# Optimization experiments

Measured on AMD Instinct MI355X. Metric: run time of the kernel, lower is better.

The kernel has to match this reference:

```python
import jax, jax.numpy as jnp
import numpy as np

T = 4096          # batch_size (time points)
C = 4096          # input_dims[1] == num_filters (channels/neurons)
FW = 64           # filter_width (temporal taps)


def setup_inputs() -> dict:
    key = jax.random.key(0)
    k1, k2, k3 = jax.random.split(key, 3)
    inputs = jax.random.normal(k1, (T, C), dtype=jnp.float32)
    weights = jax.random.uniform(k2, (FW, C), dtype=jnp.float32)
    biases = jax.random.normal(k3, (C,), dtype=jnp.float32) * 0.01
    return {"inputs": inputs, "weights": weights, "biases": biases}


def reference(inputs, weights, biases):
    # weight-norm (normalize_weights=1): per-filter L2 over taps, floored at 1e-8
    wnorms = jnp.maximum(jnp.sqrt(jnp.sum(jnp.square(weights), axis=0)), 1e-8)  # [C]
    filt = jnp.maximum(0.0, weights / wnorms)  # pos_constraint clamp, [FW, C]
    # Original does a full conv2d -> [C, T, 1, C] then takes the diagonal over
    # (batch-channel, filter-channel). Mathematically this is a per-channel
    # depthwise temporal SAME conv (cross-correlation, matching tf.nn.conv2d).
    x = inputs.T[None, :, :]            # [1, C, T]  (NCH)
    k = filt.T[:, None, :]              # [C, 1, FW] (OIH), group size 1
    pre = jax.lax.conv_general_dilated(
        x, k, window_strides=(1,), padding="SAME",
        feature_group_count=C,
        dimension_numbers=("NCH", "OIH", "NCH"))  # [1, C, T]
    # bias add; activation 'lin' = identity; ei_mask is None (num_inh=0)
    out = pre[0].T + biases[None, :]    # [T, C]
    return out
```

## Files before the change

### kernel.cpp

```cpp
#include <hip/hip_runtime.h>


#define T_DIM 4096
#define C_DIM 4096
#define PAD_L 31
#define KTILE 128

template <bool GUARD>
__device__ __forceinline__ void fir_body(const float* __restrict__ x,
                                         const float* __restrict__ w,
                                         const float* __restrict__ b,
                                         float* __restrict__ out,
                                         int c, int t0) {
    const float* __restrict__ xp = x + c;
    float* __restrict__ op = out + (long long)t0 * C_DIM + c;

    float wf[64];
    float ss = 0.0f;
#pragma unroll
    for (int f = 0; f < 64; ++f) {
        wf[f] = w[f * C_DIM + c];
        ss = fmaf(wf[f], wf[f], ss);
    }
    const float inv = 1.0f / fmaxf(sqrtf(ss), 1e-8f);
#pragma unroll
    for (int f = 0; f < 64; ++f) wf[f] = fmaxf(wf[f] * inv, 0.0f);

    const float bv = b[c];
    const int base = t0 - PAD_L;

#define LOADX(m) ((!GUARD || ((unsigned)(m) < (unsigned)T_DIM))               \
                      ? xp[(long long)(m) * C_DIM] : 0.0f)

    float xbuf[64];
#pragma unroll
    for (int i = 0; i < 64; ++i) xbuf[(i + 33) & 63] = LOADX(base + i);

    float pfA[8], pfB[8];
#pragma unroll
    for (int i = 0; i < 8; ++i) pfA[i] = LOADX(base + 64 + i);
#pragma unroll
    for (int i = 0; i < 8; ++i) pfB[i] = LOADX(base + 72 + i);

#define FIR_STEP(k, src)                                                      \
    {                                                                         \
        float a0 = bv, a1 = 0.0f, a2 = 0.0f, a3 = 0.0f;                       \
        _Pragma("unroll")                                                     \
        for (int f = 0; f < 64; f += 4) {                                     \
            a0 = fmaf(wf[f + 0], xbuf[((k) + f + 33) & 63], a0);              \
            a1 = fmaf(wf[f + 1], xbuf[((k) + f + 34) & 63], a1);              \
            a2 = fmaf(wf[f + 2], xbuf[((k) + f + 35) & 63], a2);              \
            a3 = fmaf(wf[f + 3], xbuf[((k) + f + 36) & 63], a3);              \
        }                                                                     \
        xbuf[((k) + 33) & 63] = src[(k) & 7];                                 \
        __builtin_nontemporal_store((a0 + a1) + (a2 + a3),                    \
                                    op + (long long)(kb + (k)) * C_DIM);      \
    }

#define GROUP8(gl, src)                                                       \
    FIR_STEP((gl) * 8 + 0, src) FIR_STEP((gl) * 8 + 1, src)                   \
    FIR_STEP((gl) * 8 + 2, src) FIR_STEP((gl) * 8 + 3, src)                   \
    FIR_STEP((gl) * 8 + 4, src) FIR_STEP((gl) * 8 + 5, src)                   \
    FIR_STEP((gl) * 8 + 6, src) FIR_STEP((gl) * 8 + 7, src)                   \
    _Pragma("unroll")                                                         \
    for (int i = 0; i < 8; ++i) src[i] = LOADX(base + 80 + kb + (gl) * 8 + i);

#pragma unroll 1
    for (int p = 0; p < KTILE / 64; ++p) {
        const int kb = p * 64;
        GROUP8(0, pfA) GROUP8(1, pfB) GROUP8(2, pfA) GROUP8(3, pfB)
        GROUP8(4, pfA) GROUP8(5, pfB) GROUP8(6, pfA) GROUP8(7, pfB)
    }

#undef GROUP8
#undef FIR_STEP
#undef LOADX
}

__global__ __launch_bounds__(256)
__attribute__((amdgpu_waves_per_eu(2, 2)))
void depthwise_fir_kernel(const float* __restrict__ x, const float* __restrict__ w,
                          const float* __restrict__ b, float* __restrict__ out) {
    const int c  = blockIdx.x * 256 + threadIdx.x;
    const int t0 = blockIdx.y * KTILE;
    if (blockIdx.y == 0 || blockIdx.y == gridDim.y - 1)
        fir_body<true>(x, w, b, out, c, t0);
    else
        fir_body<false>(x, w, b, out, c, t0);
}

extern "C" void kernel_launch(void* const* d_in, const int* in_sizes, int n_in,
                              void* d_out, int out_size, void* d_ws, size_t ws_size,
                              hipStream_t stream) {
    const float* x = (const float*)d_in[0];
    const float* w = (const float*)d_in[1];
    const float* b = (const float*)d_in[2];
    float* out = (float*)d_out;

    dim3 grid(C_DIM / 256, T_DIM / KTILE);
    dim3 block(256);
    hipLaunchKernelGGL(depthwise_fir_kernel, grid, block, 0, stream, x, w, b, out);
}
```

Baseline: 42.82 us.

## Restructure FIR into output-stationary 16-row tiles with chunked tap streaming

Switches from a sliding-window scheme, where each thread holds all 64 taps and a 64-entry input ring buffer across 128 time steps, to an output-stationary scheme. Each thread now keeps 16 accumulators and streams the taps in 4 chunks of 16, loading 31 inputs per chunk. The change cuts register pressure, drops the waves_per_eu cap and launches 8x more blocks to raise occupancy. In exchange, each input element is loaded about 7.75 times per output instead of about 1.5, and each block reloads and renormalizes the weights, so traffic through the caches rises sharply.

```diff
diff --git a/kernel.cpp b/kernel.cpp
--- a/kernel.cpp
+++ b/kernel.cpp
@@ -4,7 +4,9 @@
 #define T_DIM 4096
 #define C_DIM 4096
 #define PAD_L 31
-#define KTILE 128
+#define R     16
+#define CH    16
+#define NCH   4
 
 template <bool GUARD>
 __device__ __forceinline__ void fir_body(const float* __restrict__ x,
@@ -13,77 +15,62 @@
                                          float* __restrict__ out,
                                          int c, int t0) {
     const float* __restrict__ xp = x + c;
-    float* __restrict__ op = out + (long long)t0 * C_DIM + c;
+    const float* __restrict__ wp = w + c;
 
-    float wf[64];
     float ss = 0.0f;
 #pragma unroll
     for (int f = 0; f < 64; ++f) {
-        wf[f] = w[f * C_DIM + c];
-        ss = fmaf(wf[f], wf[f], ss);
+        const float v = wp[f * C_DIM];
+        ss = fmaf(v, v, ss);
     }
     const float inv = 1.0f / fmaxf(sqrtf(ss), 1e-8f);
-#pragma unroll
-    for (int f = 0; f < 64; ++f) wf[f] = fmaxf(wf[f] * inv, 0.0f);
 
     const float bv = b[c];
-    const int base = t0 - PAD_L;
+    float acc[R];
+#pragma unroll
+    for (int r = 0; r < R; ++r) acc[r] = bv;
 
-#define LOADX(m) ((!GUARD || ((unsigned)(m) < (unsigned)T_DIM))               \
-                      ? xp[(long long)(m) * C_DIM] : 0.0f)
-
-    float xbuf[64];
-#pragma unroll
-    for (int i = 0; i < 64; ++i) xbuf[(i + 33) & 63] = LOADX(base + i);
-
-    float pfA[8], pfB[8];
-#pragma unroll
-    for (int i = 0; i < 8; ++i) pfA[i] = LOADX(base + 64 + i);
-#pragma unroll
-    for (int i = 0; i < 8; ++i) pfB[i] = LOADX(base + 72 + i);
-
-#define FIR_STEP(k, src)                                                      \
+#define XSTEP(j)                                                              \
     {                                                                         \
-        float a0 = bv, a1 = 0.0f, a2 = 0.0f, a3 = 0.0f;                       \
+        const int m = xb + (j);                                               \
+        const float xv = (!GUARD || ((unsigned)m < (unsigned)T_DIM))          \
+                             ? xp[(long long)m * C_DIM] : 0.0f;               \
         _Pragma("unroll")                                                     \
-        for (int f = 0; f < 64; f += 4) {                                     \
-            a0 = fmaf(wf[f + 0], xbuf[((k) + f + 33) & 63], a0);              \
-            a1 = fmaf(wf[f + 1], xbuf[((k) + f + 34) & 63], a1);              \
-            a2 = fmaf(wf[f + 2], xbuf[((k) + f + 35) & 63], a2);              \
-            a3 = fmaf(wf[f + 3], xbuf[((k) + f + 36) & 63], a3);              \
-        }                                                                     \
-        xbuf[((k) + 33) & 63] = src[(k) & 7];                                 \
-        __builtin_nontemporal_store((a0 + a1) + (a2 + a3),                    \
-                                    op + (long long)(kb + (k)) * C_DIM);      \
+        for (int r = 0; r < R; ++r)                                           \
+            if ((j) - r >= 0 && (j) - r < CH)      \
+                acc[r] = fmaf(wf[(j) - r], xv, acc[r]);                       \
     }
 
-#define GROUP8(gl, src)                                                       \
-    FIR_STEP((gl) * 8 + 0, src) FIR_STEP((gl) * 8 + 1, src)                   \
-    FIR_STEP((gl) * 8 + 2, src) FIR_STEP((gl) * 8 + 3, src)                   \
-    FIR_STEP((gl) * 8 + 4, src) FIR_STEP((gl) * 8 + 5, src)                   \
-    FIR_STEP((gl) * 8 + 6, src) FIR_STEP((gl) * 8 + 7, src)                   \
-    _Pragma("unroll")                                                         \
-    for (int i = 0; i < 8; ++i) src[i] = LOADX(base + 80 + kb + (gl) * 8 + i);
+#pragma unroll 1
+    for (int q = 0; q < NCH; ++q) {
+        float wf[CH];
+#pragma unroll
+        for (int j = 0; j < CH; ++j)
+            wf[j] = fmaxf(wp[(q * CH + j) * C_DIM] * inv, 0.0f);
 
-#pragma unroll 1
-    for (int p = 0; p < KTILE / 64; ++p) {
-        const int kb = p * 64;
-        GROUP8(0, pfA) GROUP8(1, pfB) GROUP8(2, pfA) GROUP8(3, pfB)
-        GROUP8(4, pfA) GROUP8(5, pfB) GROUP8(6, pfA) GROUP8(7, pfB)
+        const int xb = t0 - PAD_L + q * CH;
+
+        XSTEP(0)  XSTEP(1)  XSTEP(2)  XSTEP(3)  XSTEP(4)  XSTEP(5)
+        XSTEP(6)  XSTEP(7)  XSTEP(8)  XSTEP(9)  XSTEP(10) XSTEP(11)
+        XSTEP(12) XSTEP(13) XSTEP(14) XSTEP(15) XSTEP(16) XSTEP(17)
+        XSTEP(18) XSTEP(19) XSTEP(20) XSTEP(21) XSTEP(22) XSTEP(23)
+        XSTEP(24) XSTEP(25) XSTEP(26) XSTEP(27) XSTEP(28) XSTEP(29)
+        XSTEP(30)
     }
+#undef XSTEP
 
-#undef GROUP8
-#undef FIR_STEP
-#undef LOADX
+    float* __restrict__ op = out + (long long)t0 * C_DIM + c;
+#pragma unroll
+    for (int r = 0; r < R; ++r)
+        __builtin_nontemporal_store(acc[r], op + (long long)r * C_DIM);
 }
 
 __global__ __launch_bounds__(256)
-__attribute__((amdgpu_waves_per_eu(2, 2)))
 void depthwise_fir_kernel(const float* __restrict__ x, const float* __restrict__ w,
                           const float* __restrict__ b, float* __restrict__ out) {
     const int c  = blockIdx.x * 256 + threadIdx.x;
-    const int t0 = blockIdx.y * KTILE;
-    if (blockIdx.y == 0 || blockIdx.y == gridDim.y - 1)
+    const int t0 = blockIdx.y * R;
+    if (blockIdx.y < 2 || blockIdx.y >= gridDim.y - 2)
         fir_body<true>(x, w, b, out, c, t0);
     else
         fir_body<false>(x, w, b, out, c, t0);
@@ -97,7 +84,7 @@
     const float* b = (const float*)d_in[2];
     float* out = (float*)d_out;
 
-    dim3 grid(C_DIM / 256, T_DIM / KTILE);
+    dim3 grid(C_DIM / 256, T_DIM / R);
     dim3 block(256);
     hipLaunchKernelGGL(depthwise_fir_kernel, grid, block, 0, stream, x, w, b, out);
 }
```

After: 59.25 us. 1.38x slower.

## Halve time tile, fold weight norm into output scale, single rolling prefetch

Applied to the files above, without the earlier changes.

Reduces the per-block time tile from 128 to 64 outputs, doubling the grid and making each thread fully unrolled with no outer loop. Weight normalization is refactored so the ReLU is applied to raw weights and the 1/norm scale plus bias are applied once per output via an fma, removing 64 multiplies in setup. The two 8-wide prefetch buffers become one rolling buffer refilled per step, and the waves_per_eu(2,2) hint is removed. The smaller tile raises halo reloading and weight-norm recomputation relative to useful work, in exchange for more blocks and possibly different occupancy.

```diff
diff --git a/kernel.cpp b/kernel.cpp
--- a/kernel.cpp
+++ b/kernel.cpp
@@ -4,7 +4,7 @@
 #define T_DIM 4096
 #define C_DIM 4096
 #define PAD_L 31
-#define KTILE 128
+#define KTILE 64
 
 template <bool GUARD>
 __device__ __forceinline__ void fir_body(const float* __restrict__ x,
@@ -19,14 +19,13 @@
     float ss = 0.0f;
 #pragma unroll
     for (int f = 0; f < 64; ++f) {
-        wf[f] = w[f * C_DIM + c];
-        ss = fmaf(wf[f], wf[f], ss);
+        const float wv = w[f * C_DIM + c];
+        ss = fmaf(wv, wv, ss);
+        wf[f] = fmaxf(wv, 0.0f);
     }
     const float inv = 1.0f / fmaxf(sqrtf(ss), 1e-8f);
-#pragma unroll
-    for (int f = 0; f < 64; ++f) wf[f] = fmaxf(wf[f] * inv, 0.0f);
+    const float bv = b[c];
 
-    const float bv = b[c];
     const int base = t0 - PAD_L;
 
 #define LOADX(m) ((!GUARD || ((unsigned)(m) < (unsigned)T_DIM))               \
@@ -36,15 +35,13 @@
 #pragma unroll
     for (int i = 0; i < 64; ++i) xbuf[(i + 33) & 63] = LOADX(base + i);
 
-    float pfA[8], pfB[8];
+    float pf[8];
 #pragma unroll
-    for (int i = 0; i < 8; ++i) pfA[i] = LOADX(base + 64 + i);
-#pragma unroll
-    for (int i = 0; i < 8; ++i) pfB[i] = LOADX(base + 72 + i);
+    for (int i = 0; i < 8; ++i) pf[i] = LOADX(base + 64 + i);
 
-#define FIR_STEP(k, src)                                                      \
+#define FIR_STEP(k)                                                           \
     {                                                                         \
-        float a0 = bv, a1 = 0.0f, a2 = 0.0f, a3 = 0.0f;                       \
+        float a0 = 0.0f, a1 = 0.0f, a2 = 0.0f, a3 = 0.0f;                     \
         _Pragma("unroll")                                                     \
         for (int f = 0; f < 64; f += 4) {                                     \
             a0 = fmaf(wf[f + 0], xbuf[((k) + f + 33) & 63], a0);              \
@@ -52,33 +49,27 @@
             a2 = fmaf(wf[f + 2], xbuf[((k) + f + 35) & 63], a2);              \
             a3 = fmaf(wf[f + 3], xbuf[((k) + f + 36) & 63], a3);              \
         }                                                                     \
-        xbuf[((k) + 33) & 63] = src[(k) & 7];                                 \
-        __builtin_nontemporal_store((a0 + a1) + (a2 + a3),                    \
-                                    op + (long long)(kb + (k)) * C_DIM);      \
+        xbuf[((k) + 33) & 63] = pf[(k) & 7];                                  \
+        if ((k) < KTILE - 8)                       \
+            pf[(k) & 7] = LOADX(base + 72 + (k));                             \
+        __builtin_nontemporal_store(                                          \
+            fmaf((a0 + a1) + (a2 + a3), inv, bv),                             \
+            op + (long long)(k) * C_DIM);                                     \
     }
 
-#define GROUP8(gl, src)                                                       \
-    FIR_STEP((gl) * 8 + 0, src) FIR_STEP((gl) * 8 + 1, src)                   \
-    FIR_STEP((gl) * 8 + 2, src) FIR_STEP((gl) * 8 + 3, src)                   \
-    FIR_STEP((gl) * 8 + 4, src) FIR_STEP((gl) * 8 + 5, src)                   \
-    FIR_STEP((gl) * 8 + 6, src) FIR_STEP((gl) * 8 + 7, src)                   \
-    _Pragma("unroll")                                                         \
-    for (int i = 0; i < 8; ++i) src[i] = LOADX(base + 80 + kb + (gl) * 8 + i);
+#define STEP8(b8) FIR_STEP(b8 + 0) FIR_STEP(b8 + 1) FIR_STEP(b8 + 2)          \
+                  FIR_STEP(b8 + 3) FIR_STEP(b8 + 4) FIR_STEP(b8 + 5)          \
+                  FIR_STEP(b8 + 6) FIR_STEP(b8 + 7)
 
-#pragma unroll 1
-    for (int p = 0; p < KTILE / 64; ++p) {
-        const int kb = p * 64;
-        GROUP8(0, pfA) GROUP8(1, pfB) GROUP8(2, pfA) GROUP8(3, pfB)
-        GROUP8(4, pfA) GROUP8(5, pfB) GROUP8(6, pfA) GROUP8(7, pfB)
-    }
+    STEP8(0)  STEP8(8)  STEP8(16) STEP8(24)
+    STEP8(32) STEP8(40) STEP8(48) STEP8(56)
 
-#undef GROUP8
+#undef STEP8
 #undef FIR_STEP
 #undef LOADX
 }
 
 __global__ __launch_bounds__(256)
-__attribute__((amdgpu_waves_per_eu(2, 2)))
 void depthwise_fir_kernel(const float* __restrict__ x, const float* __restrict__ w,
                           const float* __restrict__ b, float* __restrict__ out) {
     const int c  = blockIdx.x * 256 + threadIdx.x;
```

After: 43.99 us. 1.03x slower.
